# Performance work log

Measured on AMD Instinct MI355X. Metric: run time of the kernel, lower is better.

Reference implementation:

```python
import jax, jax.numpy as jnp
import numpy as np

# Static geometry (derived from calc_block_params for H=W=1024, bcount=32, k=3, s=1)
B, H, W, C = 1, 1024, 1024, 64
COUT, K, STRIDE = 64, 3, 1
BC = 32      # block count per spatial dim
BS = 34      # gather block size (bsize)
BSTR = 32    # block stride (bsize - k + stride)
BOUT = 32    # conv output block size (bsize_out)
NACT = 512
PAD = 1      # pad each side (total pad = 2 per dim)


def setup_inputs() -> dict:
    key = jax.random.key(0)
    k1, k2, k3, k4 = jax.random.split(key, 4)
    x = jax.random.normal(k1, (B, H, W, C), jnp.float32)
    # unique active block ids (flat b*BC*BC + i*BC + j), like gen_reducemask's randperm
    block_ids = jax.random.permutation(k2, B * BC * BC)[:NACT].astype(jnp.int32)
    Wk = jax.random.normal(k3, (K, K, C, COUT), jnp.float32) * 0.05
    bias = jax.random.normal(k4, (COUT,), jnp.float32) * 0.05
    return {"x": x, "block_ids": block_ids, "Wk": Wk, "bias": bias}


def _gather_blocks(xp, bidx, iidx, jidx):
    # sparse_gather: slice [BS,BS,C] block at (b, i*BSTR, j*BSTR) from padded input
    def one(bi, ii, jj):
        return jax.lax.dynamic_slice(xp, (bi, ii * BSTR, jj * BSTR, 0), (1, BS, BS, C))[0]
    return jax.vmap(one)(bidx, iidx, jidx)  # [NACT, BS, BS, C]


def reference(x, block_ids, Wk, bias):
    # F.pad with padding_params (0,0,pl,pr,pt,pb) on NHWC -> pad H and W by 1 each side
    xp = jnp.pad(x, ((0, 0), (PAD, PAD), (PAD, PAD), (0, 0)))
    bidx = block_ids // (BC * BC)
    iidx = (block_ids // BC) % BC
    jidx = block_ids % BC
    p = _gather_blocks(xp, bidx, iidx, jidx)  # [NACT, BS, BS, C]
    # dense conv on stacked active blocks (VALID, stride 1): [NACT, BOUT, BOUT, COUT]
    q = jax.lax.conv_general_dilated(
        p, Wk, window_strides=(STRIDE, STRIDE), padding='VALID',
        dimension_numbers=('NHWC', 'HWIO', 'NHWC')) + bias
    # sparse_scatter with bstride = bsize_out: non-overlapping tiling -> set semantics
    out_blocks = jnp.zeros((B * BC * BC, BOUT, BOUT, COUT), q.dtype).at[block_ids].set(q)
    y = out_blocks.reshape(B, BC, BC, BOUT, BOUT, COUT)
    y = y.transpose(0, 1, 3, 2, 4, 5).reshape(B, BC * BOUT, BC * BOUT, COUT)
    return y  # [1, 1024, 1024, 64]
```

## Files before the change

kernel.cpp:

```cpp
#include <hip/hip_runtime.h>
#include <hip/hip_bf16.h>
#include <stdint.h>


typedef __bf16 bf16x8 __attribute__((ext_vector_type(8)));
typedef float f32x16 __attribute__((ext_vector_type(16)));
typedef float f32x4 __attribute__((ext_vector_type(4)));

#define WFRAG_BYTES 73728

__device__ __forceinline__ unsigned f2bf1(float f) {
    unsigned u = __float_as_uint(f);
    u += 0x7fffu + ((u >> 16) & 1u);
    return u >> 16;
}
__device__ __forceinline__ unsigned pack2(float lo, float hi) {
    return f2bf1(lo) | (f2bf1(hi) << 16);
}

__global__ __launch_bounds__(256) void k_prep(const float* __restrict__ Wk,
                                              const int* __restrict__ ids,
                                              unsigned short* __restrict__ wfrag,
                                              int* __restrict__ flags) {
    int tid = threadIdx.x;
    if (blockIdx.x == 18) {
        #pragma unroll
        for (int i = 0; i < 4; ++i) flags[tid * 4 + i] = 0;
        __syncthreads();
        flags[ids[tid]] = 1;
        flags[ids[tid + 256]] = 1;
        return;
    }
    int t = blockIdx.x * 256 + tid;
    int lane = t & 63;
    int nt   = (t >> 6) & 1;
    int s    = (t >> 7) & 3;
    int tap  = t >> 9;
    int co = nt * 32 + (lane & 31);
    int cb = s * 16 + 8 * (lane >> 5);
    const float* wp = Wk + (tap * 64 + cb) * 64 + co;
    uint4 v;
    v.x = pack2(wp[0],   wp[64]);
    v.y = pack2(wp[128], wp[192]);
    v.z = pack2(wp[256], wp[320]);
    v.w = pack2(wp[384], wp[448]);
    ((uint4*)wfrag)[t] = v;
}

__global__ __launch_bounds__(512, 4) void k_conv(
    const float* __restrict__ x, const float* __restrict__ bias,
    const uint4* __restrict__ wfrag, const int* __restrict__ flags,
    float* __restrict__ out)
{
    __shared__ __align__(16) char lds[10 * 34 * 128];
    const int w = blockIdx.x;
    const int strip = ((w & 7) << 9) | (w >> 3);
    const int bid = strip >> 2, p = strip & 3;
    const int bi = bid >> 5, bj = bid & 31;
    const int tid = threadIdx.x;

    if (flags[bid] == 0) {
        const f32x4 z = {0.f, 0.f, 0.f, 0.f};
        for (int py = 0; py < 8; ++py) {
            f32x4* rowp = (f32x4*)(out + ((bi * 32 + p * 8 + py) * 1024 + bj * 32) * 64);
            __builtin_nontemporal_store(z, rowp + tid);
        }
        return;
    }

    const int lane = tid & 63;
    const int wv = tid >> 6;

    float4 ra[3][4];
    int rbase[3];
    int rswz[3];
    #pragma unroll
    for (int k = 0; k < 3; ++k) {
        int u = tid + k * 512;
        bool live = (k < 2) || (tid < 336);
        int q   = u & 3;
        int pix = u >> 2;
        int ly  = pix / 34;
        int lx  = pix - ly * 34;
        int yg = bi * 32 + p * 8 - 1 + ly;
        int xg = bj * 32 - 1 + lx;
        rbase[k] = pix * 128 + q * 32;
        rswz[k]  = (lx & 7) << 4;
        ra[k][0] = make_float4(0.f, 0.f, 0.f, 0.f);
        ra[k][1] = make_float4(0.f, 0.f, 0.f, 0.f);
        ra[k][2] = make_float4(0.f, 0.f, 0.f, 0.f);
        ra[k][3] = make_float4(0.f, 0.f, 0.f, 0.f);
        if (live && (unsigned)yg < 1024u && (unsigned)xg < 1024u) {
            const float4* gp = (const float4*)(x + ((yg * 1024 + xg) * 64 + q * 16));
            ra[k][0] = gp[0]; ra[k][1] = gp[1]; ra[k][2] = gp[2]; ra[k][3] = gp[3];
        }
        if (!live) rbase[k] = -1;
    }
    #pragma unroll
    for (int k = 0; k < 3; ++k) {
        if (rbase[k] < 0) continue;
        bf16x8 v0, v1;
        float4 a = ra[k][0], b = ra[k][1], c = ra[k][2], d = ra[k][3];
        v0[0] = (__bf16)a.x; v0[1] = (__bf16)a.y; v0[2] = (__bf16)a.z; v0[3] = (__bf16)a.w;
        v0[4] = (__bf16)b.x; v0[5] = (__bf16)b.y; v0[6] = (__bf16)b.z; v0[7] = (__bf16)b.w;
        v1[0] = (__bf16)c.x; v1[1] = (__bf16)c.y; v1[2] = (__bf16)c.z; v1[3] = (__bf16)c.w;
        v1[4] = (__bf16)d.x; v1[5] = (__bf16)d.y; v1[6] = (__bf16)d.z; v1[7] = (__bf16)d.w;
        *(bf16x8*)(lds + (rbase[k] ^ rswz[k]))          = v0;
        *(bf16x8*)(lds + ((rbase[k] + 16) ^ rswz[k]))   = v1;
    }
    __syncthreads();

    const float b0 = bias[lane & 31];
    const float b1 = bias[32 + (lane & 31)];
    f32x16 acc0, acc1;
    #pragma unroll
    for (int r = 0; r < 16; ++r) { acc0[r] = b0; acc1[r] = b1; }

    const int xl = lane & 31;
    const int chalf = 16 * (lane >> 5);

    #pragma unroll
    for (int kx = 0; kx < 3; ++kx) {
        int xp = xl + kx;
        int swz = (xp & 7) << 4;
        #pragma unroll
        for (int s = 0; s < 4; ++s) {
            int cbyte = s * 32 + chalf;
            bf16x8 a0 = *(const bf16x8*)(lds + ((((wv + 0) * 34 + xp) * 128 + cbyte) ^ swz));
            bf16x8 a1 = *(const bf16x8*)(lds + ((((wv + 1) * 34 + xp) * 128 + cbyte) ^ swz));
            bf16x8 a2 = *(const bf16x8*)(lds + ((((wv + 2) * 34 + xp) * 128 + cbyte) ^ swz));
            #pragma unroll
            for (int ky = 0; ky < 3; ++ky) {
                int fi = ((ky * 3 + kx) * 8 + s * 2) * 64 + lane;
                bf16x8 bf0 = *(const bf16x8*)(wfrag + fi);
                bf16x8 bf1 = *(const bf16x8*)(wfrag + fi + 64);
                bf16x8 a = (ky == 0) ? a0 : (ky == 1) ? a1 : a2;
                acc0 = __builtin_amdgcn_mfma_f32_32x32x16_bf16(a, bf0, acc0, 0, 0, 0);
                acc1 = __builtin_amdgcn_mfma_f32_32x32x16_bf16(a, bf1, acc1, 0, 0, 0);
            }
        }
    }

    const int row = bi * 32 + p * 8 + wv;
    float* orow = out + (row * 1024 + bj * 32) * 64;
    const int co = lane & 31;
    #pragma unroll
    for (int r = 0; r < 16; ++r) {
        int px = (r & 3) + 8 * (r >> 2) + 4 * (lane >> 5);
        __builtin_nontemporal_store(acc0[r], orow + px * 64 + co);
        __builtin_nontemporal_store(acc1[r], orow + px * 64 + co + 32);
    }
}

extern "C" void kernel_launch(void* const* d_in, const int* in_sizes, int n_in,
                              void* d_out, int out_size, void* d_ws, size_t ws_size,
                              hipStream_t stream) {
    const float* x    = (const float*)d_in[0];
    const int*   ids  = (const int*)d_in[1];
    const float* Wk   = (const float*)d_in[2];
    const float* bias = (const float*)d_in[3];
    float* out = (float*)d_out;

    unsigned short* wfrag = (unsigned short*)d_ws;
    int* flags = (int*)((char*)d_ws + WFRAG_BYTES);

    k_prep<<<19, 256, 0, stream>>>(Wk, ids, wfrag, flags);
    k_conv<<<4096, 512, 0, stream>>>(x, bias, (const uint4*)wfrag, flags, out);
}
```

Before: 83.90 us.

## Pair each active conv strip with an inactive zero-fill strip per workgroup

The prep kernel now builds a compact list of inactive block ids with an atomic counter. The conv kernel launches half as many workgroups. Each one zero-fills a strip of one inactive block and then convolves the matching strip of one active block, indexed through ids directly. This removes the divergence between cheap zero-fill workgroups and expensive conv workgroups and balances the work across the grid. It relies on exactly 512 active and 512 inactive blocks, which holds for this input geometry.

```diff
diff --git a/kernel.cpp b/kernel.cpp
--- a/kernel.cpp
+++ b/kernel.cpp
@@ -8,6 +8,9 @@
 typedef float f32x4 __attribute__((ext_vector_type(4)));
 
 #define WFRAG_BYTES 73728
+#define FLAGS_OFF   WFRAG_BYTES
+#define INACT_OFF   (FLAGS_OFF + 4096)
+#define CNT_OFF     (INACT_OFF + 2048)
 
 __device__ __forceinline__ unsigned f2bf1(float f) {
     unsigned u = __float_as_uint(f);
@@ -21,14 +24,26 @@
 __global__ __launch_bounds__(256) void k_prep(const float* __restrict__ Wk,
                                               const int* __restrict__ ids,
                                               unsigned short* __restrict__ wfrag,
-                                              int* __restrict__ flags) {
+                                              int* __restrict__ flags,
+                                              int* __restrict__ inact,
+                                              int* __restrict__ cnt) {
     int tid = threadIdx.x;
     if (blockIdx.x == 18) {
         #pragma unroll
         for (int i = 0; i < 4; ++i) flags[tid * 4 + i] = 0;
+        if (tid == 0) cnt[0] = 0;
         __syncthreads();
         flags[ids[tid]] = 1;
         flags[ids[tid + 256]] = 1;
+        __syncthreads();
+        #pragma unroll
+        for (int i = 0; i < 4; ++i) {
+            int b = tid * 4 + i;
+            if (flags[b] == 0) {
+                int pos = atomicAdd(cnt, 1);
+                inact[pos] = b;
+            }
+        }
         return;
     }
     int t = blockIdx.x * 256 + tid;
@@ -49,25 +64,28 @@
 
 __global__ __launch_bounds__(512, 4) void k_conv(
     const float* __restrict__ x, const float* __restrict__ bias,
-    const uint4* __restrict__ wfrag, const int* __restrict__ flags,
-    float* __restrict__ out)
+    const uint4* __restrict__ wfrag, const int* __restrict__ ids,
+    const int* __restrict__ inact, float* __restrict__ out)
 {
     __shared__ __align__(16) char lds[10 * 34 * 128];
     const int w = blockIdx.x;
-    const int strip = ((w & 7) << 9) | (w >> 3);
-    const int bid = strip >> 2, p = strip & 3;
-    const int bi = bid >> 5, bj = bid & 31;
+    const int u = ((w & 7) << 8) | (w >> 3);
+    const int li = u >> 2, p = u & 3;
     const int tid = threadIdx.x;
 
-    if (flags[bid] == 0) {
+    {
+        const int zb = inact[li];
+        const int zbi = zb >> 5, zbj = zb & 31;
         const f32x4 z = {0.f, 0.f, 0.f, 0.f};
+        #pragma unroll
         for (int py = 0; py < 8; ++py) {
-            f32x4* rowp = (f32x4*)(out + ((bi * 32 + p * 8 + py) * 1024 + bj * 32) * 64);
+            f32x4* rowp = (f32x4*)(out + ((zbi * 32 + p * 8 + py) * 1024 + zbj * 32) * 64);
             __builtin_nontemporal_store(z, rowp + tid);
         }
-        return;
     }
 
+    const int bid = ids[li];
+    const int bi = bid >> 5, bj = bid & 31;
     const int lane = tid & 63;
     const int wv = tid >> 6;
 
@@ -76,10 +94,10 @@
     int rswz[3];
     #pragma unroll
     for (int k = 0; k < 3; ++k) {
-        int u = tid + k * 512;
+        int uu = tid + k * 512;
         bool live = (k < 2) || (tid < 336);
-        int q   = u & 3;
-        int pix = u >> 2;
+        int q   = uu & 3;
+        int pix = uu >> 2;
         int ly  = pix / 34;
         int lx  = pix - ly * 34;
         int yg = bi * 32 + p * 8 - 1 + ly;
@@ -105,8 +123,8 @@
         v0[4] = (__bf16)b.x; v0[5] = (__bf16)b.y; v0[6] = (__bf16)b.z; v0[7] = (__bf16)b.w;
         v1[0] = (__bf16)c.x; v1[1] = (__bf16)c.y; v1[2] = (__bf16)c.z; v1[3] = (__bf16)c.w;
         v1[4] = (__bf16)d.x; v1[5] = (__bf16)d.y; v1[6] = (__bf16)d.z; v1[7] = (__bf16)d.w;
-        *(bf16x8*)(lds + (rbase[k] ^ rswz[k]))          = v0;
-        *(bf16x8*)(lds + ((rbase[k] + 16) ^ rswz[k]))   = v1;
+        *(bf16x8*)(lds + (rbase[k] ^ rswz[k]))        = v0;
+        *(bf16x8*)(lds + ((rbase[k] + 16) ^ rswz[k])) = v1;
     }
     __syncthreads();
 
@@ -162,8 +180,10 @@
     float* out = (float*)d_out;
 
     unsigned short* wfrag = (unsigned short*)d_ws;
-    int* flags = (int*)((char*)d_ws + WFRAG_BYTES);
+    int* flags = (int*)((char*)d_ws + FLAGS_OFF);
+    int* inact = (int*)((char*)d_ws + INACT_OFF);
+    int* cnt   = (int*)((char*)d_ws + CNT_OFF);
 
-    k_prep<<<19, 256, 0, stream>>>(Wk, ids, wfrag, flags);
-    k_conv<<<4096, 512, 0, stream>>>(x, bias, (const uint4*)wfrag, flags, out);
+    k_prep<<<19, 256, 0, stream>>>(Wk, ids, wfrag, flags, inact, cnt);
+    k_conv<<<2048, 512, 0, stream>>>(x, bias, (const uint4*)wfrag, ids, inact, out);
 }
```

Result: faster. 82.08 us (-2.2%).
